# Kernel optimization log

Measured on AMD Instinct MI355X. Metric: run time of the kernel, lower is better.

Reference implementation:

```python
import jax, jax.numpy as jnp
import numpy as np

B, L, VOCAB, EMBED, HIDDEN = 512, 256, 50000, 300, 200


def setup_inputs() -> dict:
    key = jax.random.key(0)
    ks = jax.random.split(key, 16)
    def lin(k, fan_in, fan_out):
        lim = 1.0 / np.sqrt(fan_in)
        kw, kb = jax.random.split(k)
        W = jax.random.uniform(kw, (fan_in, fan_out), jnp.float32, -lim, lim)
        b = jax.random.uniform(kb, (fan_out,), jnp.float32, -lim, lim)
        return W, b
    emb = jax.random.normal(ks[0], (VOCAB, EMBED), jnp.float32)
    W1a, b1a = lin(ks[1], EMBED, HIDDEN)
    W2a, b2a = lin(ks[2], HIDDEN, HIDDEN)
    W1c, b1c = lin(ks[3], 2 * EMBED, HIDDEN)
    W2c, b2c = lin(ks[4], HIDDEN, HIDDEN)
    W1g, b1g = lin(ks[5], 2 * HIDDEN, HIDDEN)
    W2g, b2g = lin(ks[6], HIDDEN, 2)
    s1 = jax.random.randint(ks[7], (B, L), 0, VOCAB, jnp.int32)
    s2 = jax.random.randint(ks[8], (B, L), 0, VOCAB, jnp.int32)
    len1 = jax.random.randint(ks[9], (B,), 1, L + 1, jnp.int32)
    len2 = jax.random.randint(ks[10], (B,), 1, L + 1, jnp.int32)
    return dict(emb=emb, W1a=W1a, b1a=b1a, W2a=W2a, b2a=b2a,
                W1c=W1c, b1c=b1c, W2c=W2c, b2c=b2c,
                W1g=W1g, b1g=b1g, W2g=W2g, b2g=b2g,
                s1=s1, s2=s2, len1=len1, len2=len2)


def reference(emb, W1a, b1a, W2a, b2a, W1c, b1c, W2c, b2c,
              W1g, b1g, W2g, b2g, s1, s2, len1, len2):
    relu = jax.nn.relu
    e1 = emb[s1]  # (B, L, E)
    e2 = emb[s2]
    pos = jnp.arange(L)
    mask1 = (pos[None, :] < len1[:, None]).astype(jnp.float32)  # (B, L)
    mask2 = (pos[None, :] < len2[:, None]).astype(jnp.float32)

    # Attend: shared 2-layer ReLU MLP, then bmm scores
    def attend_ff(x):
        return relu(relu(x @ W1a + b1a) @ W2a + b2a)
    h1 = attend_ff(e1)  # (B, L, H)
    h2 = attend_ff(e2)
    e = jnp.einsum('bik,bjk->bij', h1, h2)  # (B, LA, LB)

    # faithful to original: max over dim 2, broadcast along dim 1 (requires LA==LB)
    e_alpha = jnp.exp(e - jnp.max(e, axis=2)[:, None, :])
    e_alpha = e_alpha * mask1[:, :, None]
    e_alpha = e_alpha / jnp.sum(e_alpha, axis=1, keepdims=True)
    e_beta = jnp.exp(e - jnp.max(e, axis=1)[:, :, None])
    e_beta = e_beta * mask2[:, None, :]
    e_beta = e_beta / jnp.sum(e_beta, axis=2, keepdims=True)

    alphas = jnp.einsum('bij,bie->bje', e_alpha, e1) * mask2[:, :, None]  # (B, LB, E)
    betas = jnp.einsum('bij,bje->bie', e_beta, e2) * mask1[:, :, None]    # (B, LA, E)

    # Compare: shared 2-layer ReLU MLP over concatenated pairs, masked sum
    def compare_ff(x):
        return relu(relu(x @ W1c + b1c) @ W2c + b2c)
    v1 = jnp.sum(compare_ff(jnp.concatenate([e1, betas], axis=2)) * mask1[:, :, None], axis=1)  # (B, H)
    v2 = jnp.sum(compare_ff(jnp.concatenate([e2, alphas], axis=2)) * mask2[:, :, None], axis=1)

    # Aggregate
    out = relu(jnp.concatenate([v1, v2], axis=1) @ W1g + b1g) @ W2g + b2g  # (B, 2)
    return out
```

## Files before the change

kernel.cpp:

```cpp
#include <hip/hip_runtime.h>
#include <hip/hip_bf16.h>

#define DEV static __device__ __forceinline__

typedef short short8 __attribute__((ext_vector_type(8)));
typedef short short4v __attribute__((ext_vector_type(4)));
typedef float f32x4 __attribute__((ext_vector_type(4)));

#define NB 512
#define SL 256
#define ED 300
#define HD 200
#define EP 320
#define HP 224
#define TSP 232
#define PAD 40
#define GSTR 53248

#define MFMA(a,b,c) __builtin_amdgcn_mfma_f32_16x16x32_bf16(a,b,c,0,0,0)

DEV short f2b(float f){ __hip_bfloat16 h = __float2bfloat16(f); short s; __builtin_memcpy(&s,&h,2); return s; }

DEV short8 ldg_row(const short* __restrict__ Wt, int n, size_t stride, int off){
  if (n < 208) return *(const short8*)&Wt[(size_t)n*stride + off];
  short8 z = {0,0,0,0,0,0,0,0};
  return z;
}

__global__ __launch_bounds__(256) void conv_emb(const float* __restrict__ src, short* __restrict__ dst){
  size_t g = (size_t)blockIdx.x*256 + threadIdx.x;
  if (g >= (size_t)50000*EP) return;
  int row = (int)(g/EP), k = (int)(g%EP);
  dst[g] = (k<ED) ? f2b(src[(size_t)row*ED + k]) : (short)0;
}
__global__ __launch_bounds__(256) void convT_plain(const float* __restrict__ W, short* __restrict__ Wt,
                                                   int Kreal, int KP){
  int g = blockIdx.x*256 + threadIdx.x;
  if (g >= 208*KP) return;
  int n = g/KP, k = g%KP;
  float v = (n<HD && k<Kreal) ? W[(size_t)k*HD + n] : 0.f;
  Wt[g] = f2b(v);
}

__global__ __launch_bounds__(512) void mlp2(
    const short* __restrict__ embb,
    const int* __restrict__ idxA, const int* __restrict__ idxB,
    const short* __restrict__ W1t, const float* __restrict__ b1,
    const short* __restrict__ W2t, const float* __restrict__ b2,
    short* __restrict__ OutA, short* __restrict__ OutB)
{
  __shared__ __align__(16) short U[128*TSP];
  __shared__ __align__(16) short Bs[224*PAD];
  __shared__ int IdxS[128];
  const int tid=threadIdx.x, lane=tid&63, w=tid>>6, quad=lane>>4, ln=lane&15;
  const int wr=w>>1, wc=w&1;
  const int half = gridDim.x>>1;
  const int side = (blockIdx.x >= half) ? 1 : 0;
  const int row0 = (blockIdx.x - side*half)*128;
  const int* idx = side ? idxB : idxA;
  if (tid < 128) IdxS[tid] = idx[row0+tid];
  __syncthreads();

  f32x4 acc0[7], acc1[7];
  #pragma unroll
  for (int t=0;t<7;t++){ acc0[t]=(f32x4){0,0,0,0}; acc1[t]=(f32x4){0,0,0,0}; }
  const int r_ = tid>>2, c_ = tid&3;
  const size_t arow = (size_t)IdxS[r_]*EP;

  short8 aR, bR0, bR1;
  aR  = *(const short8*)&embb[arow + c_*8];
  bR0 = *(const short8*)&W1t[(size_t)r_*EP + c_*8];
  if (r_<96) bR1 = ldg_row(W1t, 128+r_, EP, c_*8);

  for (int ks=0; ks<10; ks++){
    __syncthreads();
    *(short8*)&U[r_*PAD + c_*8] = aR;
    *(short8*)&Bs[r_*PAD + c_*8] = bR0;
    if (r_<96) *(short8*)&Bs[(128+r_)*PAD + c_*8] = bR1;
    __syncthreads();
    if (ks < 9){
      const int k0 = (ks+1)*32;
      aR  = *(const short8*)&embb[arow + k0 + c_*8];
      bR0 = *(const short8*)&W1t[(size_t)r_*EP + k0 + c_*8];
      if (r_<96) bR1 = ldg_row(W1t, 128+r_, EP, k0 + c_*8);
    }
    short8 a0 = *(const short8*)&U[(wr*32+ln)*PAD + quad*8];
    short8 a1 = *(const short8*)&U[(wr*32+16+ln)*PAD + quad*8];
    #pragma unroll
    for (int tt=0; tt<7; tt++){
      short8 bb = *(const short8*)&Bs[(wc*112 + tt*16 + ln)*PAD + quad*8];
      acc0[tt] = MFMA(a0, bb, acc0[tt]);
      acc1[tt] = MFMA(a1, bb, acc1[tt]);
    }
  }
  __syncthreads();
  #pragma unroll
  for (int tt=0; tt<7; tt++){
    int col = (wc*7+tt)*16+ln;
    float bv = (col<HD) ? b1[col] : 0.f;
    #pragma unroll
    for (int r=0;r<4;r++){
      int rl = wr*32 + quad*4 + r;
      U[(rl   )*TSP + col] = f2b((col<HD) ? fmaxf(acc0[tt][r]+bv, 0.f) : 0.f);
      U[(rl+16)*TSP + col] = f2b((col<HD) ? fmaxf(acc1[tt][r]+bv, 0.f) : 0.f);
    }
    acc0[tt]=(f32x4){0,0,0,0}; acc1[tt]=(f32x4){0,0,0,0};
  }

  bR0 = *(const short8*)&W2t[(size_t)r_*HP + c_*8];
  if (r_<96) bR1 = ldg_row(W2t, 128+r_, HP, c_*8);
  for (int ks=0; ks<7; ks++){
    __syncthreads();
    *(short8*)&Bs[r_*PAD + c_*8] = bR0;
    if (r_<96) *(short8*)&Bs[(128+r_)*PAD + c_*8] = bR1;
    __syncthreads();
    if (ks < 6){
      const int k0 = (ks+1)*32;
      bR0 = *(const short8*)&W2t[(size_t)r_*HP + k0 + c_*8];
      if (r_<96) bR1 = ldg_row(W2t, 128+r_, HP, k0 + c_*8);
    }
    short8 a0 = *(const short8*)&U[(wr*32+ln)*TSP + ks*32 + quad*8];
    short8 a1 = *(const short8*)&U[(wr*32+16+ln)*TSP + ks*32 + quad*8];
    #pragma unroll
    for (int tt=0; tt<7; tt++){
      short8 bb = *(const short8*)&Bs[(wc*112 + tt*16 + ln)*PAD + quad*8];
      acc0[tt] = MFMA(a0, bb, acc0[tt]);
      acc1[tt] = MFMA(a1, bb, acc1[tt]);
    }
  }
  short* Out = side ? OutB : OutA;
  #pragma unroll
  for (int tt=0; tt<7; tt++){
    int col = (wc*7+tt)*16+ln;
    float bv = (col<HD) ? b2[col] : 0.f;
    #pragma unroll
    for (int r=0;r<4;r++){
      int rl = wr*32 + quad*4 + r;
      Out[(size_t)(row0+rl   )*HP + col] = f2b((col<HD) ? fmaxf(acc0[tt][r]+bv, 0.f) : 0.f);
      Out[(size_t)(row0+rl+16)*HP + col] = f2b((col<HD) ? fmaxf(acc1[tt][r]+bv, 0.f) : 0.f);
    }
  }
}

__global__ __launch_bounds__(256) void scores_gemm(
    const short* __restrict__ h1, const short* __restrict__ h2, float* __restrict__ e,
    unsigned* __restrict__ RmU, unsigned* __restrict__ CmU)
{
  __shared__ __align__(16) short As[64*PAD];
  __shared__ __align__(16) short Bs[64*PAD];
  const int b = blockIdx.z;
  const int i0 = blockIdx.x*64, j0 = blockIdx.y*64;
  const int tid=threadIdx.x, lane=tid&63, w=tid>>6, quad=lane>>4, ln=lane&15;
  const int r_ = tid>>2, c_ = tid&3;
  f32x4 acc[4];
  #pragma unroll
  for (int t=0;t<4;t++) acc[t]=(f32x4){0.f,0.f,0.f,0.f};
  const short* Arow = &h1[((size_t)b*SL + i0 + r_)*HP + c_*8];
  const short* Brow = &h2[((size_t)b*SL + j0 + r_)*HP + c_*8];
  short8 aR = *(const short8*)Arow;
  short8 bR = *(const short8*)Brow;
  for (int ks=0; ks<7; ks++){
    __syncthreads();
    *(short8*)&As[r_*PAD + c_*8] = aR;
    *(short8*)&Bs[r_*PAD + c_*8] = bR;
    __syncthreads();
    if (ks < 6){
      aR = *(const short8*)(Arow + (ks+1)*32);
      bR = *(const short8*)(Brow + (ks+1)*32);
    }
    short8 a = *(const short8*)&As[(w*16+ln)*PAD + quad*8];
    #pragma unroll
    for (int t=0;t<4;t++){
      short8 bb = *(const short8*)&Bs[(t*16+ln)*PAD + quad*8];
      acc[t] = MFMA(a, bb, acc[t]);
    }
  }
  #pragma unroll
  for (int t=0;t<4;t++){
    int j = j0 + t*16 + ln;
    #pragma unroll
    for (int r=0;r<4;r++){
      int i = i0 + w*16 + quad*4 + r;
      e[(size_t)b*SL*SL + (size_t)i*SL + j] = acc[t][r];
    }
  }
  #pragma unroll
  for (int r=0;r<4;r++){
    float m = fmaxf(fmaxf(acc[0][r],acc[1][r]), fmaxf(acc[2][r],acc[3][r]));
    m=fmaxf(m,__shfl_xor(m,1)); m=fmaxf(m,__shfl_xor(m,2));
    m=fmaxf(m,__shfl_xor(m,4)); m=fmaxf(m,__shfl_xor(m,8));
    if (ln==0) atomicMax(&RmU[b*SL + i0 + w*16 + quad*4 + r], __float_as_uint(m));
  }
  #pragma unroll
  for (int t=0;t<4;t++){
    float m = fmaxf(fmaxf(acc[t][0],acc[t][1]), fmaxf(acc[t][2],acc[t][3]));
    m=fmaxf(m,__shfl_xor(m,16)); m=fmaxf(m,__shfl_xor(m,32));
    if (quad==0) atomicMax(&CmU[b*SL + j0 + t*16 + ln], __float_as_uint(m));
  }
}

__global__ __launch_bounds__(256) void pwrite_k(
    const float* __restrict__ e, const unsigned* __restrict__ RmU, const unsigned* __restrict__ CmU,
    const int* __restrict__ len1, const int* __restrict__ len2,
    short* __restrict__ Pa, short* __restrict__ Pb)
{
  const int b = blockIdx.z, s = blockIdx.x, ori = blockIdx.y;
  const float* eb = e + (size_t)b*SL*SL;
  const int tid = threadIdx.x, lane = tid&63, w = tid>>6;
  if (ori == 0){
    const int l1 = len1[b], l2 = len2[b];
    if (s*64 >= l1) return;
    for (int t=0;t<16;t++){
      int i = s*64 + w*16 + t;
      if (i >= l1) break;
      float cm = __uint_as_float(CmU[b*SL+i]);
      float4 v = ((const float4*)(eb + (size_t)i*SL))[lane];
      int c0 = lane*4;
      float e0 = (c0+0<l2) ? __expf(fminf(v.x-cm,85.f)) : 0.f;
      float e1 = (c0+1<l2) ? __expf(fminf(v.y-cm,85.f)) : 0.f;
      float e2 = (c0+2<l2) ? __expf(fminf(v.z-cm,85.f)) : 0.f;
      float e3 = (c0+3<l2) ? __expf(fminf(v.w-cm,85.f)) : 0.f;
      float ss = e0+e1+e2+e3;
      ss+=__shfl_xor(ss,1); ss+=__shfl_xor(ss,2); ss+=__shfl_xor(ss,4);
      ss+=__shfl_xor(ss,8); ss+=__shfl_xor(ss,16); ss+=__shfl_xor(ss,32);
      float inv = (ss>0.f) ? 1.f/ss : 0.f;
      short4v o; o[0]=f2b(e0*inv); o[1]=f2b(e1*inv); o[2]=f2b(e2*inv); o[3]=f2b(e3*inv);
      ((short4v*)(Pb + (size_t)b*SL*SL + (size_t)i*SL))[lane] = o;
    }
  } else {
    __shared__ float Part[4][64];
    __shared__ float SaInv[64];
    __shared__ float RmS[64];
    __shared__ float Tile[64][65];
    const int l1 = len1[b], l2 = len2[b];
    const int j0 = s*64;
    if (tid < 64) RmS[tid] = __uint_as_float(RmU[b*SL + j0 + tid]);
    __syncthreads();
    {
      float sum = 0.f;
      for (int i=w; i<l1; i+=4)
        sum += __expf(fminf(eb[(size_t)i*SL + j0 + lane] - RmS[lane], 85.f));
      Part[w][lane] = sum;
    }
    __syncthreads();
    if (w==0){
      float s_ = Part[0][lane]+Part[1][lane]+Part[2][lane]+Part[3][lane];
      SaInv[lane] = (s_>0.f && (j0+lane)<l2) ? 1.f/s_ : 0.f;
    }
    __syncthreads();
    const int kmax = (l1+31)&~31;
    const int nti = (kmax+63)>>6;
    for (int ti=0; ti<nti; ti++){
      const int i0 = ti*64;
      #pragma unroll 4
      for (int it=0; it<16; it++){
        int il = it*4 + w;
        int i = i0 + il;
        float v = eb[(size_t)i*SL + j0 + lane];
        float p = (i<l1) ? __expf(fminf(v - RmS[lane],85.f))*SaInv[lane] : 0.f;
        Tile[il][lane] = p;
      }
      __syncthreads();
      {
        int jl = tid>>2, q = tid&3;
        short8 o1, o2;
        #pragma unroll
        for (int u=0;u<8;u++){
          o1[u] = f2b(Tile[q*16+u][jl]);
          o2[u] = f2b(Tile[q*16+8+u][jl]);
        }
        short* dst = Pa + (size_t)b*SL*SL + (size_t)(j0+jl)*SL + i0 + q*16;
        *(short8*)dst = o1;
        *(short8*)(dst+8) = o2;
      }
      __syncthreads();
    }
  }
}

__global__ __launch_bounds__(512) void ggemm(
    const short* __restrict__ embb, const int* __restrict__ s1c, const int* __restrict__ s2c,
    const short* __restrict__ W1bt, short* __restrict__ G1t, short* __restrict__ G2t,
    const int* __restrict__ len1, const int* __restrict__ len2, int nbc)
{
  __shared__ __align__(16) short U[208*64];
  __shared__ __align__(16) short Bs[224*PAD];
  __shared__ int IdxS[64];
  const int tid=threadIdx.x, lane=tid&63, w=tid>>6, quad=lane>>4, ln=lane&15;
  const int wr=w>>1, wc=w&1;
  const int spp = 4*nbc;
  const int side = (blockIdx.x >= spp) ? 1 : 0;
  int lin = blockIdx.x - side*spp;
  int b, rb;
  if (nbc >= 8){ int sup=lin>>5, rem=lin&31; rb=rem>>3; b=sup*8+(rem&7); }
  else { b = lin>>2; rb = lin&3; }
  const int krow0 = rb*64;
  const int lenv = (side ? len2 : len1)[b];
  if (krow0 >= lenv) return;
  const int* idx = side ? s2c : s1c;
  short* Gt = (side ? G2t : G1t) + (size_t)b*GSTR;
  if (tid < 64) IdxS[tid] = idx[b*SL + krow0 + tid];
  __syncthreads();
  f32x4 acc[7];
  #pragma unroll
  for (int t=0;t<7;t++) acc[t]=(f32x4){0,0,0,0};
  const int r_ = tid>>2, c_ = tid&3;
  const int ar = r_;
  const size_t arow = (tid<256) ? (size_t)IdxS[ar]*EP : 0;

  short8 aR, bR0, bR1;
  if (tid<256) aR = *(const short8*)&embb[arow + c_*8];
  bR0 = *(const short8*)&W1bt[(size_t)r_*EP + c_*8];
  if (r_<96) bR1 = ldg_row(W1bt, 128+r_, EP, c_*8);

  for (int ks=0; ks<10; ks++){
    __syncthreads();
    if (tid<256) *(short8*)&U[ar*PAD + c_*8] = aR;
    *(short8*)&Bs[r_*PAD + c_*8] = bR0;
    if (r_<96) *(short8*)&Bs[(128+r_)*PAD + c_*8] = bR1;
    __syncthreads();
    if (ks < 9){
      const int k0 = (ks+1)*32;
      if (tid<256) aR = *(const short8*)&embb[arow + k0 + c_*8];
      bR0 = *(const short8*)&W1bt[(size_t)r_*EP + k0 + c_*8];
      if (r_<96) bR1 = ldg_row(W1bt, 128+r_, EP, k0 + c_*8);
    }
    short8 a = *(const short8*)&U[(wr*16+ln)*PAD + quad*8];
    #pragma unroll
    for (int tt=0; tt<7; tt++){
      short8 bb = *(const short8*)&Bs[(wc*112 + tt*16 + ln)*PAD + quad*8];
      acc[tt] = MFMA(a, bb, acc[tt]);
    }
  }
  __syncthreads();
  #pragma unroll
  for (int tt=0; tt<7; tt++){
    int n = (wc*7+tt)*16+ln;
    if (n < 208){
      #pragma unroll
      for (int r=0;r<4;r++){
        int kl = wr*16 + quad*4 + r;
        U[n*64 + ((kl>>3) ^ (n&7))*8 + (kl&7)] = f2b(acc[tt][r]);
      }
    }
  }
  __syncthreads();
  #pragma unroll
  for (int it=0; it<4; it++){
    int p = it*512+tid, n = p>>3, oct = p&7;
    if (n < 208){
      short8 v = *(const short8*)&U[n*64 + (oct^(n&7))*8];
      *(short8*)&Gt[(size_t)n*SL + krow0 + oct*8] = v;
    }
  }
}

__global__ __launch_bounds__(512) void mlp2c(
    const short* __restrict__ embb,
    const int* __restrict__ s1c, const int* __restrict__ s2c,
    const short* __restrict__ Pb, const short* __restrict__ Pa,
    const short* __restrict__ G2t, const short* __restrict__ G1t,
    const short* __restrict__ W1tT, const float* __restrict__ b1,
    const short* __restrict__ W2t, const float* __restrict__ b2,
    const int* __restrict__ len1, const int* __restrict__ len2,
    float* __restrict__ v1, float* __restrict__ v2, int nbc)
{
  __shared__ __align__(16) short U[128*TSP];
  __shared__ __align__(16) short Bs[224*PAD];
  __shared__ int IdxS[128];
  const int tid=threadIdx.x, lane=tid&63, w=tid>>6, quad=lane>>4, ln=lane&15;
  const int wr=w>>1, wc=w&1;
  const int spp = 2*nbc;
  const int side = (blockIdx.x >= spp) ? 1 : 0;
  const int lin = blockIdx.x - side*spp;
  const int b = lin>>1, rb = lin&1;
  const int prow0 = rb*128;
  const int* idx = side ? s2c : s1c;
  const short* P = (side ? Pa : Pb) + (size_t)b*SL*SL;
  const short* Gt = (side ? G1t : G2t) + (size_t)b*GSTR;
  const int lenK = side ? len1[b] : len2[b];
  const int lenM = side ? len2[b] : len1[b];
  const int NK = 10 + ((lenK+31)>>5);
  float* V = side ? v2 : v1;
  if (tid < 128) IdxS[tid] = idx[b*SL + prow0 + tid];
  __syncthreads();

  f32x4 acc0[7], acc1[7];
  #pragma unroll
  for (int t=0;t<7;t++){ acc0[t]=(f32x4){0,0,0,0}; acc1[t]=(f32x4){0,0,0,0}; }
  const int r_ = tid>>2, c_ = tid&3;
  const size_t arow = (size_t)IdxS[r_]*EP;

  auto loadA = [&](int ks)->short8 {
    if (ks < 10) return *(const short8*)&embb[arow + ks*32 + c_*8];
    return *(const short8*)&P[(size_t)(prow0+r_)*SL + (ks-10)*32 + c_*8];
  };
  auto loadB = [&](int ks, int n)->short8 {
    if (n >= 208){ short8 z={0,0,0,0,0,0,0,0}; return z; }
    if (ks < 10) return *(const short8*)&W1tT[(size_t)n*EP + ks*32 + c_*8];
    return *(const short8*)&Gt[(size_t)n*SL + (ks-10)*32 + c_*8];
  };

  short8 aR, bR0, bR1;
  aR  = loadA(0);
  bR0 = loadB(0, r_);
  if (r_<96) bR1 = loadB(0, 128+r_);

  for (int ks=0; ks<NK; ks++){
    __syncthreads();
    *(short8*)&U[r_*PAD + c_*8] = aR;
    *(short8*)&Bs[r_*PAD + c_*8] = bR0;
    if (r_<96) *(short8*)&Bs[(128+r_)*PAD + c_*8] = bR1;
    __syncthreads();
    if (ks+1 < NK){
      aR  = loadA(ks+1);
      bR0 = loadB(ks+1, r_);
      if (r_<96) bR1 = loadB(ks+1, 128+r_);
    }
    short8 a0 = *(const short8*)&U[(wr*32+ln)*PAD + quad*8];
    short8 a1 = *(const short8*)&U[(wr*32+16+ln)*PAD + quad*8];
    #pragma unroll
    for (int tt=0; tt<7; tt++){
      short8 bb = *(const short8*)&Bs[(wc*112 + tt*16 + ln)*PAD + quad*8];
      acc0[tt] = MFMA(a0, bb, acc0[tt]);
      acc1[tt] = MFMA(a1, bb, acc1[tt]);
    }
  }
  __syncthreads();
  #pragma unroll
  for (int tt=0; tt<7; tt++){
    int col = (wc*7+tt)*16+ln;
    float bv = (col<HD) ? b1[col] : 0.f;
    #pragma unroll
    for (int r=0;r<4;r++){
      int rl = wr*32 + quad*4 + r;
      U[(rl   )*TSP + col] = f2b((col<HD) ? fmaxf(acc0[tt][r]+bv, 0.f) : 0.f);
      U[(rl+16)*TSP + col] = f2b((col<HD) ? fmaxf(acc1[tt][r]+bv, 0.f) : 0.f);
    }
    acc0[tt]=(f32x4){0,0,0,0}; acc1[tt]=(f32x4){0,0,0,0};
  }

  bR0 = *(const short8*)&W2t[(size_t)r_*HP + c_*8];
  if (r_<96) bR1 = ldg_row(W2t, 128+r_, HP, c_*8);
  for (int ks=0; ks<7; ks++){
    __syncthreads();
    *(short8*)&Bs[r_*PAD + c_*8] = bR0;
    if (r_<96) *(short8*)&Bs[(128+r_)*PAD + c_*8] = bR1;
    __syncthreads();
    if (ks < 6){
      const int k0 = (ks+1)*32;
      bR0 = *(const short8*)&W2t[(size_t)r_*HP + k0 + c_*8];
      if (r_<96) bR1 = ldg_row(W2t, 128+r_, HP, k0 + c_*8);
    }
    short8 a0 = *(const short8*)&U[(wr*32+ln)*TSP + ks*32 + quad*8];
    short8 a1 = *(const short8*)&U[(wr*32+16+ln)*TSP + ks*32 + quad*8];
    #pragma unroll
    for (int tt=0; tt<7; tt++){
      short8 bb = *(const short8*)&Bs[(wc*112 + tt*16 + ln)*PAD + quad*8];
      acc0[tt] = MFMA(a0, bb, acc0[tt]);
      acc1[tt] = MFMA(a1, bb, acc1[tt]);
    }
  }
  {
    const int posBase = prow0 + wr*32 + quad*4;
    #pragma unroll
    for (int tt=0; tt<7; tt++){
      int col = (wc*7+tt)*16+ln;
      float bv = (col<HD) ? b2[col] : 0.f;
      float s = 0.f;
      #pragma unroll
      for (int r=0;r<4;r++){
        float v0 = fmaxf(acc0[tt][r]+bv, 0.f); if (posBase    + r < lenM) s += v0;
        float v1_ = fmaxf(acc1[tt][r]+bv, 0.f); if (posBase+16 + r < lenM) s += v1_;
      }
      s += __shfl_xor(s,16);
      s += __shfl_xor(s,32);
      if (quad==0 && col<HD) atomicAdd(&V[b*HD+col], s);
    }
  }
}

__global__ __launch_bounds__(256) void aggregate(
    const float* __restrict__ v1, const float* __restrict__ v2,
    const float* __restrict__ W1g, const float* __restrict__ b1g,
    const float* __restrict__ W2g, const float* __restrict__ b2g,
    float* __restrict__ out)
{
  __shared__ float z[2*HD];
  __shared__ float a[HD];
  const int b = blockIdx.x, t = threadIdx.x;
  if (t < HD){ z[t] = v1[b*HD+t]; z[HD+t] = v2[b*HD+t]; }
  __syncthreads();
  if (t < HD){
    float acc = b1g[t];
    for (int k=0;k<2*HD;k++) acc += z[k]*W1g[(size_t)k*HD+t];
    a[t] = fmaxf(acc, 0.f);
  }
  __syncthreads();
  if (t < 2){
    float acc = b2g[t];
    for (int k=0;k<HD;k++) acc += a[k]*W2g[k*2+t];
    out[b*2+t] = acc;
  }
}

extern "C" void kernel_launch(void* const* d_in, const int* in_sizes, int n_in,
                              void* d_out, int out_size, void* d_ws, size_t ws_size,
                              hipStream_t stream) {
  const float* emb = (const float*)d_in[0];
  const float* W1a = (const float*)d_in[1];  const float* b1a = (const float*)d_in[2];
  const float* W2a = (const float*)d_in[3];  const float* b2a = (const float*)d_in[4];
  const float* W1c = (const float*)d_in[5];  const float* b1c = (const float*)d_in[6];
  const float* W2c = (const float*)d_in[7];  const float* b2c = (const float*)d_in[8];
  const float* W1g = (const float*)d_in[9];  const float* b1g = (const float*)d_in[10];
  const float* W2g = (const float*)d_in[11]; const float* b2g = (const float*)d_in[12];
  const int* s1 = (const int*)d_in[13];
  const int* s2 = (const int*)d_in[14];
  const int* len1 = (const int*)d_in[15];
  const int* len2 = (const int*)d_in[16];
  float* out = (float*)d_out;
  char* W = (char*)d_ws;

  float* v1    = (float*)(W);
  float* v2    = (float*)(W + 409600);
  short* embb  = (short*)(W + 819200);
  short* W1at  = (short*)(W + 32819200);
  short* W2at  = (short*)(W + 32952320);
  short* W1ctT = (short*)(W + 33045504);
  short* W1cbT = (short*)(W + 33178624);
  short* W2ct  = (short*)(W + 33311744);
  char*  C0    = W + 33404928;
  const size_t FIXED = 33404928ull;

  const size_t PERB = 526336ull;
  int nbc = NB;
  while (nbc > 1 && FIXED + (size_t)nbc*PERB > ws_size) nbc >>= 1;
  const size_t nb = (size_t)nbc;
  char* R1 = C0;
  char* R2 = C0 + nb*262144;
  char* RC = C0 + nb*524288;
  short*    h1  = (short*)(R1);
  short*    h2  = (short*)(R1 + nb*114688);
  short*    Pa  = (short*)(R1);
  short*    Pb  = (short*)(R1 + nb*131072);
  float*    e   = (float*)(R2);
  short*    G1t = (short*)(R2);
  short*    G2t = (short*)(R2 + nb*106496);
  unsigned* Rm  = (unsigned*)(RC);
  unsigned* Cm  = (unsigned*)(RC + nb*1024);

  const dim3 blk(256);
  const dim3 blk512(512);
  hipMemsetAsync(v1, 0, 2ull*NB*HD*sizeof(float), stream);
  conv_emb<<<dim3((50000*EP+255)/256), blk, 0, stream>>>(emb, embb);
  convT_plain<<<dim3((208*EP+255)/256), blk, 0, stream>>>(W1a, W1at, ED, EP);
  convT_plain<<<dim3((208*HP+255)/256), blk, 0, stream>>>(W2a, W2at, HD, HP);
  convT_plain<<<dim3((208*EP+255)/256), blk, 0, stream>>>(W1c, W1ctT, ED, EP);
  convT_plain<<<dim3((208*EP+255)/256), blk, 0, stream>>>(W1c + (size_t)ED*HD, W1cbT, ED, EP);
  convT_plain<<<dim3((208*HP+255)/256), blk, 0, stream>>>(W2c, W2ct, HD, HP);

  const int chunks = NB / nbc;
  for (int c = 0; c < chunks; c++){
    const int b0 = c * nbc;
    const int* s1c = s1 + (size_t)b0*SL;
    const int* s2c = s2 + (size_t)b0*SL;
    const int* l1c = len1 + b0;
    const int* l2c = len2 + b0;

    hipMemsetAsync(Rm, 0, (size_t)nbc*SL*8, stream);
    mlp2<<<dim3(4*nbc), blk512, 0, stream>>>(embb, s1c, s2c, W1at, b1a, W2at, b2a, h1, h2);
    scores_gemm<<<dim3(4,4,nbc), blk, 0, stream>>>(h1, h2, e, Rm, Cm);
    pwrite_k<<<dim3(4,2,nbc), blk, 0, stream>>>(e, Rm, Cm, l1c, l2c, Pa, Pb);
    ggemm<<<dim3(8*nbc), blk512, 0, stream>>>(embb, s1c, s2c, W1cbT, G1t, G2t, l1c, l2c, nbc);
    mlp2c<<<dim3(4*nbc), blk512, 0, stream>>>(embb, s1c, s2c, Pb, Pa, G2t, G1t,
                                              W1ctT, b1c, W2ct, b2c, l1c, l2c,
                                              v1 + (size_t)b0*HD, v2 + (size_t)b0*HD, nbc);
  }
  aggregate<<<dim3(NB), blk, 0, stream>>>(v1, v2, W1g, b1g, W2g, b2g, out);
}
```

Before: 654.4 us.

## Merge attend MLP and G-gemm into one launch and skip padded MFMA tiles

The attend MLP kernel and the independent G = emb·W1c_bottom GEMM now run as two block ranges of one grid, so the G work can fill the GPU alongside the MLP and one launch is removed. G buffers move to their own workspace region so they no longer alias the scores buffer, which raises per-batch workspace and may shrink the chunk count. The second wave column also skips its seventh all-padding N tile (cols 208-223), cutting MFMA and LDS work. Padding columns are zeroed explicitly and the B tile is reduced to 208 rows. The fused kernel is heterogeneous, so its register and LDS footprint is set by the larger path.

```diff
diff --git a/kernel.cpp b/kernel.cpp
--- a/kernel.cpp
+++ b/kernel.cpp
@@ -21,12 +21,6 @@
 
 DEV short f2b(float f){ __hip_bfloat16 h = __float2bfloat16(f); short s; __builtin_memcpy(&s,&h,2); return s; }
 
-DEV short8 ldg_row(const short* __restrict__ Wt, int n, size_t stride, int off){
-  if (n < 208) return *(const short8*)&Wt[(size_t)n*stride + off];
-  short8 z = {0,0,0,0,0,0,0,0};
-  return z;
-}
-
 __global__ __launch_bounds__(256) void conv_emb(const float* __restrict__ src, short* __restrict__ dst){
   size_t g = (size_t)blockIdx.x*256 + threadIdx.x;
   if (g >= (size_t)50000*EP) return;
@@ -42,102 +36,189 @@
   Wt[g] = f2b(v);
 }
 
-__global__ __launch_bounds__(512) void mlp2(
+__global__ __launch_bounds__(512) void mlp2g(
     const short* __restrict__ embb,
     const int* __restrict__ idxA, const int* __restrict__ idxB,
     const short* __restrict__ W1t, const float* __restrict__ b1,
     const short* __restrict__ W2t, const float* __restrict__ b2,
-    short* __restrict__ OutA, short* __restrict__ OutB)
+    short* __restrict__ OutA, short* __restrict__ OutB,
+    const short* __restrict__ W1bt, short* __restrict__ G1t, short* __restrict__ G2t,
+    const int* __restrict__ len1, const int* __restrict__ len2, int nbc)
 {
   __shared__ __align__(16) short U[128*TSP];
-  __shared__ __align__(16) short Bs[224*PAD];
+  __shared__ __align__(16) short Bs[208*PAD];
   __shared__ int IdxS[128];
   const int tid=threadIdx.x, lane=tid&63, w=tid>>6, quad=lane>>4, ln=lane&15;
   const int wr=w>>1, wc=w&1;
-  const int half = gridDim.x>>1;
-  const int side = (blockIdx.x >= half) ? 1 : 0;
-  const int row0 = (blockIdx.x - side*half)*128;
-  const int* idx = side ? idxB : idxA;
-  if (tid < 128) IdxS[tid] = idx[row0+tid];
-  __syncthreads();
-
-  f32x4 acc0[7], acc1[7];
-  #pragma unroll
-  for (int t=0;t<7;t++){ acc0[t]=(f32x4){0,0,0,0}; acc1[t]=(f32x4){0,0,0,0}; }
   const int r_ = tid>>2, c_ = tid&3;
-  const size_t arow = (size_t)IdxS[r_]*EP;
-
-  short8 aR, bR0, bR1;
-  aR  = *(const short8*)&embb[arow + c_*8];
-  bR0 = *(const short8*)&W1t[(size_t)r_*EP + c_*8];
-  if (r_<96) bR1 = ldg_row(W1t, 128+r_, EP, c_*8);
-
-  for (int ks=0; ks<10; ks++){
-    __syncthreads();
-    *(short8*)&U[r_*PAD + c_*8] = aR;
-    *(short8*)&Bs[r_*PAD + c_*8] = bR0;
-    if (r_<96) *(short8*)&Bs[(128+r_)*PAD + c_*8] = bR1;
-    __syncthreads();
-    if (ks < 9){
-      const int k0 = (ks+1)*32;
-      aR  = *(const short8*)&embb[arow + k0 + c_*8];
-      bR0 = *(const short8*)&W1t[(size_t)r_*EP + k0 + c_*8];
-      if (r_<96) bR1 = ldg_row(W1t, 128+r_, EP, k0 + c_*8);
-    }
-    short8 a0 = *(const short8*)&U[(wr*32+ln)*PAD + quad*8];
-    short8 a1 = *(const short8*)&U[(wr*32+16+ln)*PAD + quad*8];
+  const int NT = 7 - wc;
+
+  if ((int)blockIdx.x < 4*nbc){
+    const int half = 2*nbc;
+    const int side = ((int)blockIdx.x >= half) ? 1 : 0;
+    const int row0 = ((int)blockIdx.x - side*half)*128;
+    const int* idx = side ? idxB : idxA;
+    if (tid < 128) IdxS[tid] = idx[row0+tid];
+    __syncthreads();
+
+    f32x4 acc0[7], acc1[7];
+    #pragma unroll
+    for (int t=0;t<7;t++){ acc0[t]=(f32x4){0,0,0,0}; acc1[t]=(f32x4){0,0,0,0}; }
+    const size_t arow = (size_t)IdxS[r_]*EP;
+
+    short8 aR, bR0, bR1;
+    aR  = *(const short8*)&embb[arow + c_*8];
+    bR0 = *(const short8*)&W1t[(size_t)r_*EP + c_*8];
+    if (r_<80) bR1 = *(const short8*)&W1t[(size_t)(128+r_)*EP + c_*8];
+
+    for (int ks=0; ks<10; ks++){
+      __syncthreads();
+      *(short8*)&U[r_*PAD + c_*8] = aR;
+      *(short8*)&Bs[r_*PAD + c_*8] = bR0;
+      if (r_<80) *(short8*)&Bs[(128+r_)*PAD + c_*8] = bR1;
+      __syncthreads();
+      if (ks < 9){
+        const int k0 = (ks+1)*32;
+        aR  = *(const short8*)&embb[arow + k0 + c_*8];
+        bR0 = *(const short8*)&W1t[(size_t)r_*EP + k0 + c_*8];
+        if (r_<80) bR1 = *(const short8*)&W1t[(size_t)(128+r_)*EP + k0 + c_*8];
+      }
+      short8 a0 = *(const short8*)&U[(wr*32+ln)*PAD + quad*8];
+      short8 a1 = *(const short8*)&U[(wr*32+16+ln)*PAD + quad*8];
+      #pragma unroll
+      for (int tt=0; tt<7; tt++){
+        if (tt < NT){
+          short8 bb = *(const short8*)&Bs[(wc*112 + tt*16 + ln)*PAD + quad*8];
+          acc0[tt] = MFMA(a0, bb, acc0[tt]);
+          acc1[tt] = MFMA(a1, bb, acc1[tt]);
+        }
+      }
+    }
+    __syncthreads();
     #pragma unroll
     for (int tt=0; tt<7; tt++){
-      short8 bb = *(const short8*)&Bs[(wc*112 + tt*16 + ln)*PAD + quad*8];
-      acc0[tt] = MFMA(a0, bb, acc0[tt]);
-      acc1[tt] = MFMA(a1, bb, acc1[tt]);
-    }
-  }
-  __syncthreads();
-  #pragma unroll
-  for (int tt=0; tt<7; tt++){
-    int col = (wc*7+tt)*16+ln;
-    float bv = (col<HD) ? b1[col] : 0.f;
-    #pragma unroll
-    for (int r=0;r<4;r++){
-      int rl = wr*32 + quad*4 + r;
-      U[(rl   )*TSP + col] = f2b((col<HD) ? fmaxf(acc0[tt][r]+bv, 0.f) : 0.f);
-      U[(rl+16)*TSP + col] = f2b((col<HD) ? fmaxf(acc1[tt][r]+bv, 0.f) : 0.f);
-    }
-    acc0[tt]=(f32x4){0,0,0,0}; acc1[tt]=(f32x4){0,0,0,0};
-  }
-
-  bR0 = *(const short8*)&W2t[(size_t)r_*HP + c_*8];
-  if (r_<96) bR1 = ldg_row(W2t, 128+r_, HP, c_*8);
-  for (int ks=0; ks<7; ks++){
-    __syncthreads();
-    *(short8*)&Bs[r_*PAD + c_*8] = bR0;
-    if (r_<96) *(short8*)&Bs[(128+r_)*PAD + c_*8] = bR1;
-    __syncthreads();
-    if (ks < 6){
-      const int k0 = (ks+1)*32;
-      bR0 = *(const short8*)&W2t[(size_t)r_*HP + k0 + c_*8];
-      if (r_<96) bR1 = ldg_row(W2t, 128+r_, HP, k0 + c_*8);
-    }
-    short8 a0 = *(const short8*)&U[(wr*32+ln)*TSP + ks*32 + quad*8];
-    short8 a1 = *(const short8*)&U[(wr*32+16+ln)*TSP + ks*32 + quad*8];
+      if (tt < NT){
+        int col = (wc*7+tt)*16+ln;
+        float bv = (col<HD) ? b1[col] : 0.f;
+        #pragma unroll
+        for (int r=0;r<4;r++){
+          int rl = wr*32 + quad*4 + r;
+          U[(rl   )*TSP + col] = f2b((col<HD) ? fmaxf(acc0[tt][r]+bv, 0.f) : 0.f);
+          U[(rl+16)*TSP + col] = f2b((col<HD) ? fmaxf(acc1[tt][r]+bv, 0.f) : 0.f);
+        }
+      }
+      acc0[tt]=(f32x4){0,0,0,0}; acc1[tt]=(f32x4){0,0,0,0};
+    }
+    { short4v z4 = {0,0,0,0};
+      *(short4v*)&U[(tid>>2)*TSP + 208 + (tid&3)*4] = z4; }
+
+    bR0 = *(const short8*)&W2t[(size_t)r_*HP + c_*8];
+    if (r_<80) bR1 = *(const short8*)&W2t[(size_t)(128+r_)*HP + c_*8];
+    for (int ks=0; ks<7; ks++){
+      __syncthreads();
+      *(short8*)&Bs[r_*PAD + c_*8] = bR0;
+      if (r_<80) *(short8*)&Bs[(128+r_)*PAD + c_*8] = bR1;
+      __syncthreads();
+      if (ks < 6){
+        const int k0 = (ks+1)*32;
+        bR0 = *(const short8*)&W2t[(size_t)r_*HP + k0 + c_*8];
+        if (r_<80) bR1 = *(const short8*)&W2t[(size_t)(128+r_)*HP + k0 + c_*8];
+      }
+      short8 a0 = *(const short8*)&U[(wr*32+ln)*TSP + ks*32 + quad*8];
+      short8 a1 = *(const short8*)&U[(wr*32+16+ln)*TSP + ks*32 + quad*8];
+      #pragma unroll
+      for (int tt=0; tt<7; tt++){
+        if (tt < NT){
+          short8 bb = *(const short8*)&Bs[(wc*112 + tt*16 + ln)*PAD + quad*8];
+          acc0[tt] = MFMA(a0, bb, acc0[tt]);
+          acc1[tt] = MFMA(a1, bb, acc1[tt]);
+        }
+      }
+    }
+    short* Out = side ? OutB : OutA;
     #pragma unroll
     for (int tt=0; tt<7; tt++){
-      short8 bb = *(const short8*)&Bs[(wc*112 + tt*16 + ln)*PAD + quad*8];
-      acc0[tt] = MFMA(a0, bb, acc0[tt]);
-      acc1[tt] = MFMA(a1, bb, acc1[tt]);
-    }
-  }
-  short* Out = side ? OutB : OutA;
-  #pragma unroll
-  for (int tt=0; tt<7; tt++){
-    int col = (wc*7+tt)*16+ln;
-    float bv = (col<HD) ? b2[col] : 0.f;
-    #pragma unroll
-    for (int r=0;r<4;r++){
-      int rl = wr*32 + quad*4 + r;
-      Out[(size_t)(row0+rl   )*HP + col] = f2b((col<HD) ? fmaxf(acc0[tt][r]+bv, 0.f) : 0.f);
-      Out[(size_t)(row0+rl+16)*HP + col] = f2b((col<HD) ? fmaxf(acc1[tt][r]+bv, 0.f) : 0.f);
+      if (tt < NT){
+        int col = (wc*7+tt)*16+ln;
+        float bv = (col<HD) ? b2[col] : 0.f;
+        #pragma unroll
+        for (int r=0;r<4;r++){
+          int rl = wr*32 + quad*4 + r;
+          Out[(size_t)(row0+rl   )*HP + col] = f2b((col<HD) ? fmaxf(acc0[tt][r]+bv, 0.f) : 0.f);
+          Out[(size_t)(row0+rl+16)*HP + col] = f2b((col<HD) ? fmaxf(acc1[tt][r]+bv, 0.f) : 0.f);
+        }
+      }
+    }
+    { short4v z4 = {0,0,0,0};
+      *(short4v*)&Out[(size_t)(row0+(tid>>2))*HP + 208 + (tid&3)*4] = z4; }
+
+  } else {
+    const int gb = (int)blockIdx.x - 4*nbc;
+    const int spp = 4*nbc;
+    const int side = (gb >= spp) ? 1 : 0;
+    int lin = gb - side*spp;
+    int b, rb;
+    if (nbc >= 8){ int sup=lin>>5, rem=lin&31; rb=rem>>3; b=sup*8+(rem&7); }
+    else { b = lin>>2; rb = lin&3; }
+    const int krow0 = rb*64;
+    const int lenv = (side ? len2 : len1)[b];
+    if (krow0 >= lenv) return;
+    const int* idx = side ? idxB : idxA;
+    short* Gt = (side ? G2t : G1t) + (size_t)b*GSTR;
+    if (tid < 64) IdxS[tid] = idx[b*SL + krow0 + tid];
+    __syncthreads();
+    f32x4 acc[7];
+    #pragma unroll
+    for (int t=0;t<7;t++) acc[t]=(f32x4){0,0,0,0};
+    const size_t arow = (tid<256) ? (size_t)IdxS[r_]*EP : 0;
+    const int gwr = w>>1;
+
+    short8 aR, bR0, bR1;
+    if (tid<256) aR = *(const short8*)&embb[arow + c_*8];
+    bR0 = *(const short8*)&W1bt[(size_t)r_*EP + c_*8];
+    if (r_<80) bR1 = *(const short8*)&W1bt[(size_t)(128+r_)*EP + c_*8];
+
+    for (int ks=0; ks<10; ks++){
+      __syncthreads();
+      if (tid<256) *(short8*)&U[r_*PAD + c_*8] = aR;
+      *(short8*)&Bs[r_*PAD + c_*8] = bR0;
+      if (r_<80) *(short8*)&Bs[(128+r_)*PAD + c_*8] = bR1;
+      __syncthreads();
+      if (ks < 9){
+        const int k0 = (ks+1)*32;
+        if (tid<256) aR = *(const short8*)&embb[arow + k0 + c_*8];
+        bR0 = *(const short8*)&W1bt[(size_t)r_*EP + k0 + c_*8];
+        if (r_<80) bR1 = *(const short8*)&W1bt[(size_t)(128+r_)*EP + k0 + c_*8];
+      }
+      short8 a = *(const short8*)&U[(gwr*16+ln)*PAD + quad*8];
+      #pragma unroll
+      for (int tt=0; tt<7; tt++){
+        if (tt < NT){
+          short8 bb = *(const short8*)&Bs[(wc*112 + tt*16 + ln)*PAD + quad*8];
+          acc[tt] = MFMA(a, bb, acc[tt]);
+        }
+      }
+    }
+    __syncthreads();
+    #pragma unroll
+    for (int tt=0; tt<7; tt++){
+      if (tt < NT){
+        int n = (wc*7+tt)*16+ln;
+        #pragma unroll
+        for (int r=0;r<4;r++){
+          int kl = gwr*16 + quad*4 + r;
+          U[n*64 + ((kl>>3) ^ (n&7))*8 + (kl&7)] = f2b(acc[tt][r]);
+        }
+      }
+    }
+    __syncthreads();
+    #pragma unroll
+    for (int it=0; it<4; it++){
+      int p = it*512+tid, n = p>>3, oct = p&7;
+      if (n < 208){
+        short8 v = *(const short8*)&U[n*64 + (oct^(n&7))*8];
+        *(short8*)&Gt[(size_t)n*SL + krow0 + oct*8] = v;
+      }
     }
   }
 }
@@ -278,83 +359,6 @@
   }
 }
 
-__global__ __launch_bounds__(512) void ggemm(
-    const short* __restrict__ embb, const int* __restrict__ s1c, const int* __restrict__ s2c,
-    const short* __restrict__ W1bt, short* __restrict__ G1t, short* __restrict__ G2t,
-    const int* __restrict__ len1, const int* __restrict__ len2, int nbc)
-{
-  __shared__ __align__(16) short U[208*64];
-  __shared__ __align__(16) short Bs[224*PAD];
-  __shared__ int IdxS[64];
-  const int tid=threadIdx.x, lane=tid&63, w=tid>>6, quad=lane>>4, ln=lane&15;
-  const int wr=w>>1, wc=w&1;
-  const int spp = 4*nbc;
-  const int side = (blockIdx.x >= spp) ? 1 : 0;
-  int lin = blockIdx.x - side*spp;
-  int b, rb;
-  if (nbc >= 8){ int sup=lin>>5, rem=lin&31; rb=rem>>3; b=sup*8+(rem&7); }
-  else { b = lin>>2; rb = lin&3; }
-  const int krow0 = rb*64;
-  const int lenv = (side ? len2 : len1)[b];
-  if (krow0 >= lenv) return;
-  const int* idx = side ? s2c : s1c;
-  short* Gt = (side ? G2t : G1t) + (size_t)b*GSTR;
-  if (tid < 64) IdxS[tid] = idx[b*SL + krow0 + tid];
-  __syncthreads();
-  f32x4 acc[7];
-  #pragma unroll
-  for (int t=0;t<7;t++) acc[t]=(f32x4){0,0,0,0};
-  const int r_ = tid>>2, c_ = tid&3;
-  const int ar = r_;
-  const size_t arow = (tid<256) ? (size_t)IdxS[ar]*EP : 0;
-
-  short8 aR, bR0, bR1;
-  if (tid<256) aR = *(const short8*)&embb[arow + c_*8];
-  bR0 = *(const short8*)&W1bt[(size_t)r_*EP + c_*8];
-  if (r_<96) bR1 = ldg_row(W1bt, 128+r_, EP, c_*8);
-
-  for (int ks=0; ks<10; ks++){
-    __syncthreads();
-    if (tid<256) *(short8*)&U[ar*PAD + c_*8] = aR;
-    *(short8*)&Bs[r_*PAD + c_*8] = bR0;
-    if (r_<96) *(short8*)&Bs[(128+r_)*PAD + c_*8] = bR1;
-    __syncthreads();
-    if (ks < 9){
-      const int k0 = (ks+1)*32;
-      if (tid<256) aR = *(const short8*)&embb[arow + k0 + c_*8];
-      bR0 = *(const short8*)&W1bt[(size_t)r_*EP + k0 + c_*8];
-      if (r_<96) bR1 = ldg_row(W1bt, 128+r_, EP, k0 + c_*8);
-    }
-    short8 a = *(const short8*)&U[(wr*16+ln)*PAD + quad*8];
-    #pragma unroll
-    for (int tt=0; tt<7; tt++){
-      short8 bb = *(const short8*)&Bs[(wc*112 + tt*16 + ln)*PAD + quad*8];
-      acc[tt] = MFMA(a, bb, acc[tt]);
-    }
-  }
-  __syncthreads();
-  #pragma unroll
-  for (int tt=0; tt<7; tt++){
-    int n = (wc*7+tt)*16+ln;
-    if (n < 208){
-      #pragma unroll
-      for (int r=0;r<4;r++){
-        int kl = wr*16 + quad*4 + r;
-        U[n*64 + ((kl>>3) ^ (n&7))*8 + (kl&7)] = f2b(acc[tt][r]);
-      }
-    }
-  }
-  __syncthreads();
-  #pragma unroll
-  for (int it=0; it<4; it++){
-    int p = it*512+tid, n = p>>3, oct = p&7;
-    if (n < 208){
-      short8 v = *(const short8*)&U[n*64 + (oct^(n&7))*8];
-      *(short8*)&Gt[(size_t)n*SL + krow0 + oct*8] = v;
-    }
-  }
-}
-
 __global__ __launch_bounds__(512) void mlp2c(
     const short* __restrict__ embb,
     const int* __restrict__ s1c, const int* __restrict__ s2c,
@@ -366,13 +370,14 @@
     float* __restrict__ v1, float* __restrict__ v2, int nbc)
 {
   __shared__ __align__(16) short U[128*TSP];
-  __shared__ __align__(16) short Bs[224*PAD];
+  __shared__ __align__(16) short Bs[208*PAD];
   __shared__ int IdxS[128];
   const int tid=threadIdx.x, lane=tid&63, w=tid>>6, quad=lane>>4, ln=lane&15;
   const int wr=w>>1, wc=w&1;
+  const int NT = 7 - wc;
   const int spp = 2*nbc;
-  const int side = (blockIdx.x >= spp) ? 1 : 0;
-  const int lin = blockIdx.x - side*spp;
+  const int side = ((int)blockIdx.x >= spp) ? 1 : 0;
+  const int lin = (int)blockIdx.x - side*spp;
   const int b = lin>>1, rb = lin&1;
   const int prow0 = rb*128;
   const int* idx = side ? s2c : s1c;
@@ -396,7 +401,6 @@
     return *(const short8*)&P[(size_t)(prow0+r_)*SL + (ks-10)*32 + c_*8];
   };
   auto loadB = [&](int ks, int n)->short8 {
-    if (n >= 208){ short8 z={0,0,0,0,0,0,0,0}; return z; }
     if (ks < 10) return *(const short8*)&W1tT[(size_t)n*EP + ks*32 + c_*8];
     return *(const short8*)&Gt[(size_t)n*SL + (ks-10)*32 + c_*8];
   };
@@ -404,78 +408,88 @@
   short8 aR, bR0, bR1;
   aR  = loadA(0);
   bR0 = loadB(0, r_);
-  if (r_<96) bR1 = loadB(0, 128+r_);
+  if (r_<80) bR1 = loadB(0, 128+r_);
 
   for (int ks=0; ks<NK; ks++){
     __syncthreads();
     *(short8*)&U[r_*PAD + c_*8] = aR;
     *(short8*)&Bs[r_*PAD + c_*8] = bR0;
-    if (r_<96) *(short8*)&Bs[(128+r_)*PAD + c_*8] = bR1;
+    if (r_<80) *(short8*)&Bs[(128+r_)*PAD + c_*8] = bR1;
     __syncthreads();
     if (ks+1 < NK){
       aR  = loadA(ks+1);
       bR0 = loadB(ks+1, r_);
-      if (r_<96) bR1 = loadB(ks+1, 128+r_);
+      if (r_<80) bR1 = loadB(ks+1, 128+r_);
     }
     short8 a0 = *(const short8*)&U[(wr*32+ln)*PAD + quad*8];
     short8 a1 = *(const short8*)&U[(wr*32+16+ln)*PAD + quad*8];
     #pragma unroll
     for (int tt=0; tt<7; tt++){
-      short8 bb = *(const short8*)&Bs[(wc*112 + tt*16 + ln)*PAD + quad*8];
-      acc0[tt] = MFMA(a0, bb, acc0[tt]);
-      acc1[tt] = MFMA(a1, bb, acc1[tt]);
+      if (tt < NT){
+        short8 bb = *(const short8*)&Bs[(wc*112 + tt*16 + ln)*PAD + quad*8];
+        acc0[tt] = MFMA(a0, bb, acc0[tt]);
+        acc1[tt] = MFMA(a1, bb, acc1[tt]);
+      }
     }
   }
   __syncthreads();
   #pragma unroll
   for (int tt=0; tt<7; tt++){
-    int col = (wc*7+tt)*16+ln;
-    float bv = (col<HD) ? b1[col] : 0.f;
-    #pragma unroll
-    for (int r=0;r<4;r++){
-      int rl = wr*32 + quad*4 + r;
-      U[(rl   )*TSP + col] = f2b((col<HD) ? fmaxf(acc0[tt][r]+bv, 0.f) : 0.f);
-      U[(rl+16)*TSP + col] = f2b((col<HD) ? fmaxf(acc1[tt][r]+bv, 0.f) : 0.f);
+    if (tt < NT){
+      int col = (wc*7+tt)*16+ln;
+      float bv = (col<HD) ? b1[col] : 0.f;
+      #pragma unroll
+      for (int r=0;r<4;r++){
+        int rl = wr*32 + quad*4 + r;
+        U[(rl   )*TSP + col] = f2b((col<HD) ? fmaxf(acc0[tt][r]+bv, 0.f) : 0.f);
+        U[(rl+16)*TSP + col] = f2b((col<HD) ? fmaxf(acc1[tt][r]+bv, 0.f) : 0.f);
+      }
     }
     acc0[tt]=(f32x4){0,0,0,0}; acc1[tt]=(f32x4){0,0,0,0};
   }
+  { short4v z4 = {0,0,0,0};
+    *(short4v*)&U[(tid>>2)*TSP + 208 + (tid&3)*4] = z4; }
 
   bR0 = *(const short8*)&W2t[(size_t)r_*HP + c_*8];
-  if (r_<96) bR1 = ldg_row(W2t, 128+r_, HP, c_*8);
+  if (r_<80) bR1 = *(const short8*)&W2t[(size_t)(128+r_)*HP + c_*8];
   for (int ks=0; ks<7; ks++){
     __syncthreads();
     *(short8*)&Bs[r_*PAD + c_*8] = bR0;
-    if (r_<96) *(short8*)&Bs[(128+r_)*PAD + c_*8] = bR1;
+    if (r_<80) *(short8*)&Bs[(128+r_)*PAD + c_*8] = bR1;
     __syncthreads();
     if (ks < 6){
       const int k0 = (ks+1)*32;
       bR0 = *(const short8*)&W2t[(size_t)r_*HP + k0 + c_*8];
-      if (r_<96) bR1 = ldg_row(W2t, 128+r_, HP, k0 + c_*8);
+      if (r_<80) bR1 = *(const short8*)&W2t[(size_t)(128+r_)*HP + k0 + c_*8];
     }
     short8 a0 = *(const short8*)&U[(wr*32+ln)*TSP + ks*32 + quad*8];
     short8 a1 = *(const short8*)&U[(wr*32+16+ln)*TSP + ks*32 + quad*8];
     #pragma unroll
     for (int tt=0; tt<7; tt++){
-      short8 bb = *(const short8*)&Bs[(wc*112 + tt*16 + ln)*PAD + quad*8];
-      acc0[tt] = MFMA(a0, bb, acc0[tt]);
-      acc1[tt] = MFMA(a1, bb, acc1[tt]);
+      if (tt < NT){
+        short8 bb = *(const short8*)&Bs[(wc*112 + tt*16 + ln)*PAD + quad*8];
+        acc0[tt] = MFMA(a0, bb, acc0[tt]);
+        acc1[tt] = MFMA(a1, bb, acc1[tt]);
+      }
     }
   }
   {
     const int posBase = prow0 + wr*32 + quad*4;
     #pragma unroll
     for (int tt=0; tt<7; tt++){
-      int col = (wc*7+tt)*16+ln;
-      float bv = (col<HD) ? b2[col] : 0.f;
-      float s = 0.f;
-      #pragma unroll
-      for (int r=0;r<4;r++){
-        float v0 = fmaxf(acc0[tt][r]+bv, 0.f); if (posBase    + r < lenM) s += v0;
-        float v1_ = fmaxf(acc1[tt][r]+bv, 0.f); if (posBase+16 + r < lenM) s += v1_;
-      }
-      s += __shfl_xor(s,16);
-      s += __shfl_xor(s,32);
-      if (quad==0 && col<HD) atomicAdd(&V[b*HD+col], s);
+      if (tt < NT){
+        int col = (wc*7+tt)*16+ln;
+        float bv = (col<HD) ? b2[col] : 0.f;
+        float s = 0.f;
+        #pragma unroll
+        for (int r=0;r<4;r++){
+          float v0 = fmaxf(acc0[tt][r]+bv, 0.f); if (posBase    + r < lenM) s += v0;
+          float v1_ = fmaxf(acc1[tt][r]+bv, 0.f); if (posBase+16 + r < lenM) s += v1_;
+        }
+        s += __shfl_xor(s,16);
+        s += __shfl_xor(s,32);
+        if (quad==0 && col<HD) atomicAdd(&V[b*HD+col], s);
+      }
     }
   }
 }
@@ -532,20 +546,21 @@
   char*  C0    = W + 33404928;
   const size_t FIXED = 33404928ull;
 
-  const size_t PERB = 526336ull;
+  const size_t PERB = 739328ull;
   int nbc = NB;
   while (nbc > 1 && FIXED + (size_t)nbc*PERB > ws_size) nbc >>= 1;
   const size_t nb = (size_t)nbc;
   char* R1 = C0;
   char* R2 = C0 + nb*262144;
-  char* RC = C0 + nb*524288;
+  char* R3 = C0 + nb*524288;
+  char* RC = C0 + nb*737280;
   short*    h1  = (short*)(R1);
   short*    h2  = (short*)(R1 + nb*114688);
   short*    Pa  = (short*)(R1);
   short*    Pb  = (short*)(R1 + nb*131072);
   float*    e   = (float*)(R2);
-  short*    G1t = (short*)(R2);
-  short*    G2t = (short*)(R2 + nb*106496);
+  short*    G1t = (short*)(R3);
+  short*    G2t = (short*)(R3 + nb*106496);
   unsigned* Rm  = (unsigned*)(RC);
   unsigned* Cm  = (unsigned*)(RC + nb*1024);
 
@@ -568,10 +583,10 @@
     const int* l2c = len2 + b0;
 
     hipMemsetAsync(Rm, 0, (size_t)nbc*SL*8, stream);
-    mlp2<<<dim3(4*nbc), blk512, 0, stream>>>(embb, s1c, s2c, W1at, b1a, W2at, b2a, h1, h2);
+    mlp2g<<<dim3(12*nbc), blk512, 0, stream>>>(embb, s1c, s2c, W1at, b1a, W2at, b2a, h1, h2,
+                                               W1cbT, G1t, G2t, l1c, l2c, nbc);
     scores_gemm<<<dim3(4,4,nbc), blk, 0, stream>>>(h1, h2, e, Rm, Cm);
     pwrite_k<<<dim3(4,2,nbc), blk, 0, stream>>>(e, Rm, Cm, l1c, l2c, Pa, Pb);
-    ggemm<<<dim3(8*nbc), blk512, 0, stream>>>(embb, s1c, s2c, W1cbT, G1t, G2t, l1c, l2c, nbc);
     mlp2c<<<dim3(4*nbc), blk512, 0, stream>>>(embb, s1c, s2c, Pb, Pa, G2t, G1t,
                                               W1ctT, b1c, W2ct, b2c, l1c, l2c,
                                               v1 + (size_t)b0*HD, v2 + (size_t)b0*HD, nbc);
```

After: 645.1 us. No clear change (-1.4%).
